# Kernel tuning notes

Hardware: AMD Instinct MI355X
Metric: run time of the kernel (lower is better)

Reference implementation:

```python
import jax, jax.numpy as jnp
import numpy as np

DIM = 2048
NUM_EXPERTS = 8
N_TOKENS = 8192
SPARSITY = 0.8  # sparsity_constraint parameter (used only to derive static k)
K = max(1, int(SPARSITY * NUM_EXPERTS))  # = 6


def setup_inputs() -> dict:
    key = jax.random.key(0)
    ks = jax.random.split(key, 5)
    scale = 1.0 / np.sqrt(DIM)
    x = jax.random.normal(ks[0], (N_TOKENS, DIM), dtype=jnp.float32)
    Wg = jax.random.uniform(ks[1], (NUM_EXPERTS, DIM), jnp.float32, -scale, scale)
    bg = jax.random.uniform(ks[2], (NUM_EXPERTS,), jnp.float32, -scale, scale)
    We = jax.random.uniform(ks[3], (NUM_EXPERTS, DIM, DIM), jnp.float32, -scale, scale)
    be = jax.random.uniform(ks[4], (NUM_EXPERTS, DIM), jnp.float32, -scale, scale)
    return {"x": x, "Wg": Wg, "bg": bg, "We": We, "be": be}


def reference(x, Wg, bg, We, be):
    # gate scores: [N, E]
    gate_scores = x @ Wg.T + bg
    # top-k expert indices per token: [N, K]
    _, topk_idx = jax.lax.top_k(gate_scores, K)
    # mask[n, e] = expert e is among token n's top-k: [N, E]
    mask = jnp.any(topk_idx[:, :, None] == jnp.arange(NUM_EXPERTS)[None, None, :], axis=1)
    # all expert outputs: [N, E, D]  (We is [E, out, in]; Linear = x @ W.T + b)
    expert_out = jnp.einsum('nd,efd->nef', x, We) + be[None, :, :]
    # combine: unweighted sum of selected experts' outputs (no gate weighting in source)
    out = jnp.sum(expert_out * mask[:, :, None].astype(x.dtype), axis=1)
    return out
```

## Files before the change

kernel.cpp:

```cpp
#include <hip/hip_runtime.h>
#include <hip/hip_bf16.h>
#include <stdint.h>

#define DIM 2048
#define NEXP 8
#define NTOK 8192
#define KSEL 6
#define NPAIR 28
#define SLOTS 92

typedef short bf16x8 __attribute__((ext_vector_type(8)));
typedef float f32x4 __attribute__((ext_vector_type(4)));
typedef const __attribute__((address_space(1))) unsigned int GU32;
typedef __attribute__((address_space(3))) unsigned int LU32;

static constexpr int PA[NPAIR] = {0,0,0,0,0,0,0,1,1,1,1,1,1,2,2,2,2,2,3,3,3,3,4,4,4,5,5,6};
static constexpr int PB[NPAIR] = {1,2,3,4,5,6,7,2,3,4,5,6,7,3,4,5,6,7,4,5,6,7,5,6,7,6,7,7};

__device__ __forceinline__ unsigned short f2b(float f) {
  union { float f; uint32_t u; } v; v.f = f;
  return (unsigned short)((v.u + 0x7fffu + ((v.u >> 16) & 1u)) >> 16);
}

__global__ void zero_cnt_kernel(int* cnt) {
  if (threadIdx.x < NPAIR) cnt[threadIdx.x] = 0;
}

__global__ __launch_bounds__(256) void gate_kernel(
    const float* __restrict__ x, const float* __restrict__ Wg,
    const float* __restrict__ bg, unsigned short* __restrict__ xB,
    int* __restrict__ pid) {
  int t = threadIdx.x;
  int w = t >> 6, l = t & 63;
  int n = blockIdx.x * 4 + w;
  const float* xr = x + (size_t)n * DIM;
  float xv[32];
#pragma unroll
  for (int j = 0; j < 8; ++j) {
    float4 v = *(const float4*)(xr + 4 * l + 256 * j);
    xv[4 * j + 0] = v.x; xv[4 * j + 1] = v.y;
    xv[4 * j + 2] = v.z; xv[4 * j + 3] = v.w;
  }
  unsigned short* xbr = xB + (size_t)n * DIM;
#pragma unroll
  for (int j = 0; j < 8; ++j) {
    ushort4 o;
    o.x = f2b(xv[4 * j + 0]); o.y = f2b(xv[4 * j + 1]);
    o.z = f2b(xv[4 * j + 2]); o.w = f2b(xv[4 * j + 3]);
    *(ushort4*)(xbr + 4 * l + 256 * j) = o;
  }
  float sc[NEXP];
#pragma unroll
  for (int e = 0; e < NEXP; ++e) {
    const float* wr = Wg + e * DIM;
    float s = 0.f;
#pragma unroll
    for (int j = 0; j < 8; ++j) {
      float4 v = *(const float4*)(wr + 4 * l + 256 * j);
      s += xv[4 * j + 0] * v.x + xv[4 * j + 1] * v.y +
           xv[4 * j + 2] * v.z + xv[4 * j + 3] * v.w;
    }
#pragma unroll
    for (int off = 32; off > 0; off >>= 1) s += __shfl_xor(s, off, 64);
    sc[e] = s + bg[e];
  }
  if (l == 0) {
    int ex0 = -1, ex1 = -1;
#pragma unroll
    for (int e = 0; e < NEXP; ++e) {
      int rank = 0;
#pragma unroll
      for (int j = 0; j < NEXP; ++j)
        rank += (sc[j] > sc[e]) || (sc[j] == sc[e] && j < e);
      if (rank >= KSEL) { if (ex0 < 0) ex0 = e; else if (ex1 < 0) ex1 = e; }
    }
    pid[n] = ex0 * (15 - ex0) / 2 + (ex1 - ex0 - 1);
  }
}

__global__ __launch_bounds__(256) void bucket_kernel(
    const int* __restrict__ pid, int* __restrict__ cnt, int* __restrict__ list) {
  __shared__ int lcnt[NPAIR];
  __shared__ int gbase[NPAIR];
  int t = threadIdx.x;
  if (t < NPAIR) lcnt[t] = 0;
  __syncthreads();
  int base = blockIdx.x * 2048;
  int p[8], lp[8];
#pragma unroll
  for (int j = 0; j < 8; ++j) {
    int n = base + t + 256 * j;
    p[j] = pid[n];
    lp[j] = atomicAdd(&lcnt[p[j]], 1);
  }
  __syncthreads();
  if (t < NPAIR) gbase[t] = atomicAdd(&cnt[t], lcnt[t]);
  __syncthreads();
#pragma unroll
  for (int j = 0; j < 8; ++j) {
    int n = base + t + 256 * j;
    list[p[j] * NTOK + gbase[p[j]] + lp[j]] = n;
  }
}

__global__ void tilemap_kernel(const int* __restrict__ cnt, int* __restrict__ tileBase) {
  if (threadIdx.x == 0) {
    int s = 0;
    for (int p = 0; p < NPAIR; ++p) { tileBase[p] = s; s += (cnt[p] + 127) >> 7; }
    tileBase[NPAIR] = s;
  }
}

__global__ __launch_bounds__(256) void biaspair_kernel(
    const float* __restrict__ be, float* __restrict__ biasPair) {
  int f = blockIdx.x * 256 + threadIdx.x;
  float v[NEXP]; float s = 0.f;
#pragma unroll
  for (int e = 0; e < NEXP; ++e) { v[e] = be[e * DIM + f]; s += v[e]; }
#pragma unroll
  for (int pp = 0; pp < NPAIR; ++pp)
    biasPair[pp * DIM + f] = s - v[PA[pp]] - v[PB[pp]];
}

__global__ __launch_bounds__(256) void pairw_kernel(
    const float* __restrict__ We, unsigned short* __restrict__ Wp,
    int fbase, int frows) {
  size_t pos = ((size_t)blockIdx.x * 256 + threadIdx.x) * 4;
  size_t src = (size_t)fbase * DIM + pos;
  float4 v[NEXP];
  float sx = 0.f, sy = 0.f, sz = 0.f, sw = 0.f;
#pragma unroll
  for (int e = 0; e < NEXP; ++e) {
    v[e] = *(const float4*)(We + (size_t)e * DIM * DIM + src);
    sx += v[e].x; sy += v[e].y; sz += v[e].z; sw += v[e].w;
  }
  size_t chunk = (size_t)frows * DIM;
#pragma unroll
  for (int pp = 0; pp < NPAIR; ++pp) {
    int a = PA[pp], b = PB[pp];
    ushort4 o;
    o.x = f2b(sx - v[a].x - v[b].x);
    o.y = f2b(sy - v[a].y - v[b].y);
    o.z = f2b(sz - v[a].z - v[b].z);
    o.w = f2b(sw - v[a].w - v[b].w);
    *(ushort4*)(Wp + (size_t)pp * chunk + pos) = o;
  }
}

__global__ __launch_bounds__(256, 3) void gemm_pair(
    const unsigned short* __restrict__ A, const unsigned short* __restrict__ Wp,
    const int* __restrict__ cnt, const int* __restrict__ list,
    const int* __restrict__ tileBase, const float* __restrict__ biasPair,
    float* __restrict__ out, int fbase, int frows) {
  __shared__ unsigned short sA[128 * 64];
  __shared__ unsigned short sB[128 * 64];
  __shared__ int sRows[128];
  int slot = blockIdx.y, ft = blockIdx.x;
  if (slot >= tileBase[NPAIR]) return;
  int p = 0;
  while (p + 1 < NPAIR && tileBase[p + 1] <= slot) ++p;
  int c = cnt[p];
  int m0 = (slot - tileBase[p]) * 128;

  int t = threadIdx.x;
  int w = t >> 6, l = t & 63;
  int wm = w & 1, wn = w >> 1;
  int quad = l >> 4, lr = l & 15;
  int cs = (l & 7) ^ ((l >> 3) & 7);

  if (t < 128) {
    int idx = m0 + t;
    if (idx >= c) idx = c - 1;
    sRows[t] = list[p * NTOK + idx];
  }
  __syncthreads();

  size_t rowOffA[4], rowOffB[4];
#pragma unroll
  for (int i = 0; i < 4; ++i)
    rowOffA[i] = (size_t)sRows[i * 32 + w * 8 + (l >> 3)] * DIM;
  const unsigned short* Bb =
      Wp + (size_t)p * frows * DIM + (size_t)ft * 128 * DIM;
#pragma unroll
  for (int i = 0; i < 4; ++i)
    rowOffB[i] = (size_t)(i * 32 + w * 8 + (l >> 3)) * DIM;

  f32x4 acc[4][4];
#pragma unroll
  for (int mi = 0; mi < 4; ++mi)
#pragma unroll
    for (int ni = 0; ni < 4; ++ni) {
      acc[mi][ni][0] = 0.f; acc[mi][ni][1] = 0.f;
      acc[mi][ni][2] = 0.f; acc[mi][ni][3] = 0.f;
    }

  for (int k0 = 0; k0 < DIM; k0 += 64) {
#pragma unroll
    for (int i = 0; i < 4; ++i) {
      __builtin_amdgcn_global_load_lds((GU32*)(A + rowOffA[i] + k0 + cs * 8),
          (LU32*)(sA + (i * 32 + w * 8) * 64), 16, 0, 0);
      __builtin_amdgcn_global_load_lds((GU32*)(Bb + rowOffB[i] + k0 + cs * 8),
          (LU32*)(sB + (i * 32 + w * 8) * 64), 16, 0, 0);
    }
    __syncthreads();
#pragma unroll
    for (int ks = 0; ks < 2; ++ks) {
      bf16x8 aF[4], bF[4];
#pragma unroll
      for (int mi = 0; mi < 4; ++mi)
        aF[mi] = *(const bf16x8*)(sA + (wm * 64 + mi * 16 + lr) * 64 +
                                  (((ks << 2) | quad) ^ (lr & 7)) * 8);
#pragma unroll
      for (int ni = 0; ni < 4; ++ni)
        bF[ni] = *(const bf16x8*)(sB + (wn * 64 + ni * 16 + lr) * 64 +
                                  (((ks << 2) | quad) ^ (lr & 7)) * 8);
#pragma unroll
      for (int mi = 0; mi < 4; ++mi)
#pragma unroll
        for (int ni = 0; ni < 4; ++ni)
          acc[mi][ni] = __builtin_amdgcn_mfma_f32_16x16x32_bf16(aF[mi], bF[ni], acc[mi][ni], 0, 0, 0);
    }
    __syncthreads();
  }

  int f0 = fbase + ft * 128;
  float bb[4];
#pragma unroll
  for (int ni = 0; ni < 4; ++ni)
    bb[ni] = biasPair[p * DIM + f0 + wn * 64 + ni * 16 + lr];
#pragma unroll
  for (int mi = 0; mi < 4; ++mi) {
#pragma unroll
    for (int i = 0; i < 4; ++i) {
      int lrow = wm * 64 + mi * 16 + quad * 4 + i;
      if (m0 + lrow < c) {
        float* orow = out + (size_t)sRows[lrow] * DIM + f0;
#pragma unroll
        for (int ni = 0; ni < 4; ++ni)
          orow[wn * 64 + ni * 16 + lr] = acc[mi][ni][i] + bb[ni];
      }
    }
  }
}

extern "C" void kernel_launch(void* const* d_in, const int* in_sizes, int n_in,
                              void* d_out, int out_size, void* d_ws, size_t ws_size,
                              hipStream_t stream) {
  const float* x  = (const float*)d_in[0];
  const float* Wg = (const float*)d_in[1];
  const float* bg = (const float*)d_in[2];
  const float* We = (const float*)d_in[3];
  const float* be = (const float*)d_in[4];
  float* out = (float*)d_out;

  char* ws = (char*)d_ws;
  unsigned short* xB = (unsigned short*)ws; ws += (size_t)NTOK * DIM * 2;
  int* pid = (int*)ws;          ws += (size_t)NTOK * 4;
  int* cnt = (int*)ws;          ws += 128;
  int* tileBase = (int*)ws;     ws += 128;
  int* list = (int*)ws;         ws += (size_t)NPAIR * NTOK * 4;
  float* biasPair = (float*)ws; ws += (size_t)NPAIR * DIM * 4;
  unsigned short* Wp = (unsigned short*)ws;

  size_t avail = ws_size - (size_t)(ws - (char*)d_ws);
  int NR = 1;
  while (NR < 16 && (size_t)NPAIR * DIM * (size_t)(DIM / NR) * 2 > avail) NR <<= 1;
  int frows = DIM / NR;

  zero_cnt_kernel<<<1, 64, 0, stream>>>(cnt);
  gate_kernel<<<NTOK / 4, 256, 0, stream>>>(x, Wg, bg, xB, pid);
  bucket_kernel<<<4, 256, 0, stream>>>(pid, cnt, list);
  tilemap_kernel<<<1, 64, 0, stream>>>(cnt, tileBase);
  biaspair_kernel<<<DIM / 256, 256, 0, stream>>>(be, biasPair);
  for (int r = 0; r < NR; ++r) {
    int fbase = r * frows;
    pairw_kernel<<<(frows * DIM) / 1024, 256, 0, stream>>>(We, Wp, fbase, frows);
    gemm_pair<<<dim3(frows / 128, SLOTS), 256, 0, stream>>>(
        xB, Wp, cnt, list, tileBase, biasPair, out, fbase, frows);
  }
}
```

Before: 464.3 us.

## Build pair weights on the fly in GEMM from fp32 sum and expert slices

Result: slower. 602.9 us (+29.8%).

```diff
diff --git a/kernel.cpp b/kernel.cpp
--- a/kernel.cpp
+++ b/kernel.cpp
@@ -10,6 +10,7 @@
 #define SLOTS 92
 
 typedef short bf16x8 __attribute__((ext_vector_type(8)));
+typedef unsigned short u16x8 __attribute__((ext_vector_type(8)));
 typedef float f32x4 __attribute__((ext_vector_type(4)));
 typedef const __attribute__((address_space(1))) unsigned int GU32;
 typedef __attribute__((address_space(3))) unsigned int LU32;
@@ -122,36 +123,25 @@
     biasPair[pp * DIM + f] = s - v[PA[pp]] - v[PB[pp]];
 }
 
-__global__ __launch_bounds__(256) void pairw_kernel(
-    const float* __restrict__ We, unsigned short* __restrict__ Wp,
-    int fbase, int frows) {
-  size_t pos = ((size_t)blockIdx.x * 256 + threadIdx.x) * 4;
-  size_t src = (size_t)fbase * DIM + pos;
-  float4 v[NEXP];
+__global__ __launch_bounds__(256) void wsum_kernel(
+    const float* __restrict__ We, float* __restrict__ Wsumf) {
+  size_t p = ((size_t)blockIdx.x * 256 + threadIdx.x) * 4;
   float sx = 0.f, sy = 0.f, sz = 0.f, sw = 0.f;
 #pragma unroll
   for (int e = 0; e < NEXP; ++e) {
-    v[e] = *(const float4*)(We + (size_t)e * DIM * DIM + src);
-    sx += v[e].x; sy += v[e].y; sz += v[e].z; sw += v[e].w;
-  }
-  size_t chunk = (size_t)frows * DIM;
-#pragma unroll
-  for (int pp = 0; pp < NPAIR; ++pp) {
-    int a = PA[pp], b = PB[pp];
-    ushort4 o;
-    o.x = f2b(sx - v[a].x - v[b].x);
-    o.y = f2b(sy - v[a].y - v[b].y);
-    o.z = f2b(sz - v[a].z - v[b].z);
-    o.w = f2b(sw - v[a].w - v[b].w);
-    *(ushort4*)(Wp + (size_t)pp * chunk + pos) = o;
-  }
+    float4 v = *(const float4*)(We + (size_t)e * DIM * DIM + p);
+    sx += v.x; sy += v.y; sz += v.z; sw += v.w;
+  }
+  float4 o; o.x = sx; o.y = sy; o.z = sz; o.w = sw;
+  *(float4*)(Wsumf + p) = o;
 }
 
 __global__ __launch_bounds__(256, 3) void gemm_pair(
-    const unsigned short* __restrict__ A, const unsigned short* __restrict__ Wp,
+    const unsigned short* __restrict__ A, const float* __restrict__ Wsumf,
+    const float* __restrict__ We,
     const int* __restrict__ cnt, const int* __restrict__ list,
     const int* __restrict__ tileBase, const float* __restrict__ biasPair,
-    float* __restrict__ out, int fbase, int frows) {
+    float* __restrict__ out) {
   __shared__ unsigned short sA[128 * 64];
   __shared__ unsigned short sB[128 * 64];
   __shared__ int sRows[128];
@@ -161,6 +151,12 @@
   while (p + 1 < NPAIR && tileBase[p + 1] <= slot) ++p;
   int c = cnt[p];
   int m0 = (slot - tileBase[p]) * 128;
+  if (m0 >= c) return;
+  int pv = p, a = 0;
+  while (pv >= 7 - a) { pv -= 7 - a; ++a; }
+  int b = a + 1 + pv;
+  const float* Wea = We + (size_t)a * DIM * DIM;
+  const float* Web = We + (size_t)b * DIM * DIM;
 
   int t = threadIdx.x;
   int w = t >> 6, l = t & 63;
@@ -175,15 +171,14 @@
   }
   __syncthreads();
 
-  size_t rowOffA[4], rowOffB[4];
-#pragma unroll
-  for (int i = 0; i < 4; ++i)
+  size_t rowOffA[4], bOff[4];
+  int ldsRow[4];
+#pragma unroll
+  for (int i = 0; i < 4; ++i) {
     rowOffA[i] = (size_t)sRows[i * 32 + w * 8 + (l >> 3)] * DIM;
-  const unsigned short* Bb =
-      Wp + (size_t)p * frows * DIM + (size_t)ft * 128 * DIM;
-#pragma unroll
-  for (int i = 0; i < 4; ++i)
-    rowOffB[i] = (size_t)(i * 32 + w * 8 + (l >> 3)) * DIM;
+    bOff[i] = (size_t)(ft * 128 + i * 32 + w * 8 + (l >> 3)) * DIM + cs * 8;
+    ldsRow[i] = (i * 32 + w * 8) * 64 + l * 8;
+  }
 
   f32x4 acc[4][4];
 #pragma unroll
@@ -196,11 +191,23 @@
 
   for (int k0 = 0; k0 < DIM; k0 += 64) {
 #pragma unroll
-    for (int i = 0; i < 4; ++i) {
+    for (int i = 0; i < 4; ++i)
       __builtin_amdgcn_global_load_lds((GU32*)(A + rowOffA[i] + k0 + cs * 8),
           (LU32*)(sA + (i * 32 + w * 8) * 64), 16, 0, 0);
-      __builtin_amdgcn_global_load_lds((GU32*)(Bb + rowOffB[i] + k0 + cs * 8),
-          (LU32*)(sB + (i * 32 + w * 8) * 64), 16, 0, 0);
+#pragma unroll
+    for (int i = 0; i < 4; ++i) {
+      const float* pS = Wsumf + bOff[i] + k0;
+      const float* pa = Wea + bOff[i] + k0;
+      const float* pb = Web + bOff[i] + k0;
+      float4 s0 = *(const float4*)(pS);     float4 s1 = *(const float4*)(pS + 4);
+      float4 a0 = *(const float4*)(pa);     float4 a1 = *(const float4*)(pa + 4);
+      float4 b0 = *(const float4*)(pb);     float4 b1 = *(const float4*)(pb + 4);
+      u16x8 v;
+      v[0] = f2b(s0.x - a0.x - b0.x); v[1] = f2b(s0.y - a0.y - b0.y);
+      v[2] = f2b(s0.z - a0.z - b0.z); v[3] = f2b(s0.w - a0.w - b0.w);
+      v[4] = f2b(s1.x - a1.x - b1.x); v[5] = f2b(s1.y - a1.y - b1.y);
+      v[6] = f2b(s1.z - a1.z - b1.z); v[7] = f2b(s1.w - a1.w - b1.w);
+      *(u16x8*)(sB + ldsRow[i]) = v;
     }
     __syncthreads();
 #pragma unroll
@@ -223,7 +230,7 @@
     __syncthreads();
   }
 
-  int f0 = fbase + ft * 128;
+  int f0 = ft * 128;
   float bb[4];
 #pragma unroll
   for (int ni = 0; ni < 4; ++ni)
@@ -260,22 +267,14 @@
   int* tileBase = (int*)ws;     ws += 128;
   int* list = (int*)ws;         ws += (size_t)NPAIR * NTOK * 4;
   float* biasPair = (float*)ws; ws += (size_t)NPAIR * DIM * 4;
-  unsigned short* Wp = (unsigned short*)ws;
-
-  size_t avail = ws_size - (size_t)(ws - (char*)d_ws);
-  int NR = 1;
-  while (NR < 16 && (size_t)NPAIR * DIM * (size_t)(DIM / NR) * 2 > avail) NR <<= 1;
-  int frows = DIM / NR;
+  float* Wsumf = (float*)ws;    ws += (size_t)DIM * DIM * 4;
 
   zero_cnt_kernel<<<1, 64, 0, stream>>>(cnt);
   gate_kernel<<<NTOK / 4, 256, 0, stream>>>(x, Wg, bg, xB, pid);
   bucket_kernel<<<4, 256, 0, stream>>>(pid, cnt, list);
   tilemap_kernel<<<1, 64, 0, stream>>>(cnt, tileBase);
   biaspair_kernel<<<DIM / 256, 256, 0, stream>>>(be, biasPair);
-  for (int r = 0; r < NR; ++r) {
-    int fbase = r * frows;
-    pairw_kernel<<<(frows * DIM) / 1024, 256, 0, stream>>>(We, Wp, fbase, frows);
-    gemm_pair<<<dim3(frows / 128, SLOTS), 256, 0, stream>>>(
-        xB, Wp, cnt, list, tileBase, biasPair, out, fbase, frows);
-  }
-}
+  wsum_kernel<<<(DIM * DIM) / 1024, 256, 0, stream>>>(We, Wsumf);
+  gemm_pair<<<dim3(DIM / 128, SLOTS), 256, 0, stream>>>(
+      xB, Wsumf, We, cnt, list, tileBase, biasPair, out);
+}
```
